# Performance work log

Measured on AMD Instinct MI355X. Metric: run time of the kernel, lower is better.

The kernel has to match this reference:

```python
import jax, jax.numpy as jnp
import numpy as np

# Model config (matches init_kwargs)
DAG_DEPTH = 16
HIDDEN = 2048
B, T = 4, 4096
N = DAG_DEPTH                 # total_nodes
INIT_SLOTS = DAG_DEPTH // 2   # initial slots
INTER = DAG_DEPTH // 2        # intermediate slots / scan steps
LOG_CLAMP = 23.026
SIGN_TEMP = 1e-4


def _xavier(k, shape):
    fan_out, fan_in = shape
    lim = np.sqrt(6.0 / (fan_in + fan_out)).astype(np.float32)
    return jax.random.uniform(k, shape, jnp.float32, -lim, lim)


def setup_inputs() -> dict:
    key = jax.random.key(0)
    k0, k1, k2, k3 = jax.random.split(key, 4)
    return {
        "hidden": jax.random.normal(k0, (B, T, HIDDEN), jnp.float32),
        "W_init": _xavier(k1, (2 * N, HIDDEN)),
        "b_init": jnp.zeros((2 * N,), jnp.float32),
        "W_op": _xavier(k2, (INTER * N, HIDDEN)),
        "b_op": jnp.zeros((INTER * N,), jnp.float32),
        "W_gate": _xavier(k3, (INTER, HIDDEN)),
        "b_gate": jnp.zeros((INTER,), jnp.float32),
    }


def reference(hidden, W_init, b_init, W_op, b_op, W_gate, b_gate):
    Bb, Tt, H = hidden.shape
    # --- plan predictor ---
    init_raw = jnp.einsum('bth,oh->bto', hidden, W_init) + b_init        # (B,T,2N)
    V_mag = jnp.abs(init_raw[..., :N])                                   # (B,T,N)
    V_sign = jnp.tanh(init_raw[..., N:])                                 # (B,T,N)
    O = (jnp.einsum('bth,oh->bto', hidden, W_op) + b_op).reshape(Bb, Tt, INTER, N)
    G = jax.nn.sigmoid(jnp.einsum('bth,oh->bto', hidden, W_gate) + b_gate)  # (B,T,INTER)

    # --- sequential DAG execution (fixed INTER steps, vectorized over B,T) ---
    # NOTE: torch casts to float64 (float32 on mps); here we compute in float32,
    # identical math modulo precision (jax x64 is disabled by default).
    pos = jnp.arange(N)
    for step in range(INTER):
        valid = INIT_SLOTS + step
        mask = (pos < valid).astype(hidden.dtype)                        # causal mask over nodes
        O_s = O[:, :, step, :] * mask                                    # (B,T,N)
        G_s = G[:, :, step:step + 1]                                     # (B,T,1)
        signed = V_sign * V_mag
        log_mag = jnp.log(jnp.clip(V_mag, 1e-12))
        mixed = log_mag * (1.0 - G_s) + signed * G_s
        R = jnp.sum(O_s * mixed, axis=-1, keepdims=True)                 # (B,T,1)
        lin_sign = jnp.tanh(R / SIGN_TEMP)
        sign_prod = jnp.prod(V_sign * (jnp.abs(O_s) + 1.0), axis=-1, keepdims=True)
        log_sign = jnp.tanh(sign_prod / SIGN_TEMP)
        Vs_new = G_s * lin_sign + (1.0 - G_s) * log_sign
        Vm_new = G_s * jnp.abs(R) + (1.0 - G_s) * jnp.exp(jnp.clip(R, None, LOG_CLAMP))
        idx = INIT_SLOTS + step
        V_mag = V_mag.at[:, :, idx].set(Vm_new[..., 0])
        V_sign = V_sign.at[:, :, idx].set(Vs_new[..., 0])

    return V_sign[:, :, -1] * V_mag[:, :, -1]                            # (B,T)
```

## Files before the change

### kernel.cpp

```cpp
#include <hip/hip_runtime.h>
#include <math.h>

#define HID    2048
#define NROW   16384
#define NCOL   168
#define BM     64
#define KSTEPS 64
#define NCHUNK 33
#define NELEM  2112
#define BUFB   33792
#define CPD    172
#define NSLOT  16
#define NSTEP  8

typedef short short8 __attribute__((ext_vector_type(8)));
typedef float f32x4  __attribute__((ext_vector_type(4)));
typedef unsigned int u32x4 __attribute__((ext_vector_type(4)));

static __device__ __forceinline__ unsigned pack_hi(unsigned u0, unsigned u1) {
  return __builtin_amdgcn_perm(u1, u0, 0x07060302u);
}

struct Planes { u32x4 p1, p2, p3; };
static __device__ __forceinline__ Planes split8(const float* x) {
  Planes P;
  #pragma unroll
  for (int q = 0; q < 4; ++q) {
    float x0 = x[2*q], x1 = x[2*q+1];
    unsigned u0 = __float_as_uint(x0), u1 = __float_as_uint(x1);
    P.p1[q] = pack_hi(u0, u1);
    float r0 = x0 - __uint_as_float(u0 & 0xFFFF0000u);
    float r1 = x1 - __uint_as_float(u1 & 0xFFFF0000u);
    unsigned v0 = __float_as_uint(r0), v1 = __float_as_uint(r1);
    P.p2[q] = pack_hi(v0, v1);
    float s0 = r0 - __uint_as_float(v0 & 0xFFFF0000u);
    float s1 = r1 - __uint_as_float(v1 & 0xFFFF0000u);
    P.p3[q] = pack_hi(__float_as_uint(s0), __float_as_uint(s1));
  }
  return P;
}

static __device__ __forceinline__ void loadA8(const float* p, float* x) {
  float4 a = *(const float4*)p;
  float4 b = *(const float4*)(p + 4);
  x[0]=a.x; x[1]=a.y; x[2]=a.z; x[3]=a.w;
  x[4]=b.x; x[5]=b.y; x[6]=b.z; x[7]=b.w;
}

static __device__ __forceinline__ f32x4 mf(short8 a, short8 b, f32x4 c) {
  return __builtin_amdgcn_mfma_f32_16x16x32_bf16(a, b, c, 0, 0, 0);
}

static __device__ __forceinline__ void gld_lds16(const void* g, void* l) {
  __builtin_amdgcn_global_load_lds(
      (const __attribute__((address_space(1))) unsigned int*)g,
      (__attribute__((address_space(3))) unsigned int*)l, 16, 0, 0);
}

__global__ void prep_b(const float* __restrict__ Wi, const float* __restrict__ Wo,
                       const float* __restrict__ Wg, u32x4* __restrict__ wsB) {
  int bid  = blockIdx.x;
  int kidx = bid / 11;
  int nt   = bid - kidx * 11;
  int l    = threadIdx.x;
  int col  = nt * 16 + (l & 15);
  int k0   = kidx * 32 + (l >> 4) * 8;

  float x[8];
  if (col < NCOL) {
    const float* wr = (col < 32)  ? (Wi + (size_t)col * HID)
                    : (col < 160) ? (Wo + (size_t)(col - 32) * HID)
                                  : (Wg + (size_t)(col - 160) * HID);
    loadA8(wr + k0, x);
  } else {
    #pragma unroll
    for (int i = 0; i < 8; ++i) x[i] = 0.f;
  }
  Planes P = split8(x);
  size_t base = (size_t)kidx * NELEM + (nt * 3) * 64 + l;
  wsB[base]       = P.p1;
  wsB[base + 64]  = P.p2;
  wsB[base + 128] = P.p3;
}

__global__ __launch_bounds__(512, 2)
void dag_main(const float* __restrict__ hidden, const u32x4* __restrict__ wsB,
              const float* __restrict__ b_init, const float* __restrict__ b_op,
              const float* __restrict__ b_gate, float* __restrict__ out)
{
  __shared__ __align__(16) char smem[2 * BUFB];

  const int tid = threadIdx.x;
  const int l   = tid & 63;
  const int w   = tid >> 6;
  const int wm  = w >> 2;
  const int wn  = w & 3;
  const int row0 = blockIdx.x * BM;
  const int r   = l & 15;
  const int kg  = l >> 4;

  const float* ap0 = hidden + (size_t)(row0 + wm * 32 + r) * HID + kg * 8;
  const float* ap1 = ap0 + (size_t)16 * HID;

  const u32x4* bsrc = wsB + tid;
  char* wbase = smem + w * 1024;
  const char* brd0 = smem + (wn * 9 * 64 + l) * 16;

  f32x4 acc[2][3];
  const f32x4 zf = {0.f, 0.f, 0.f, 0.f};
  #pragma unroll
  for (int mt = 0; mt < 2; ++mt)
    #pragma unroll
    for (int j = 0; j < 3; ++j) acc[mt][j] = zf;

  float xs0[8], xs1[8];

#define STAGE(t_, sel_) do {                                   \
    const u32x4* s_ = bsrc + (size_t)NELEM * (t_);             \
    char* d_ = wbase + (sel_) * BUFB;                          \
    gld_lds16(s_,        d_);                                  \
    gld_lds16(s_ + 512,  d_ + 8192);                           \
    gld_lds16(s_ + 1024, d_ + 16384);                          \
    gld_lds16(s_ + 1536, d_ + 24576);                          \
    if (w == 0) gld_lds16(s_ + 2048, d_ + 32768 - w * 1024);   \
  } while (0)

  STAGE(0, 0);
  loadA8(ap0, xs0);
  loadA8(ap1, xs1);
  __syncthreads();

  for (int t = 0; t < KSTEPS; ++t) {
    Planes PA0 = split8(xs0);
    Planes PA1 = split8(xs1);
    short8 a0p1 = __builtin_bit_cast(short8, PA0.p1);
    short8 a0p2 = __builtin_bit_cast(short8, PA0.p2);
    short8 a0p3 = __builtin_bit_cast(short8, PA0.p3);
    short8 a1p1 = __builtin_bit_cast(short8, PA1.p1);
    short8 a1p2 = __builtin_bit_cast(short8, PA1.p2);
    short8 a1p3 = __builtin_bit_cast(short8, PA1.p3);

    if (t + 1 < KSTEPS) {
      STAGE(t + 1, (t + 1) & 1);
      loadA8(ap0 + (t + 1) * 32, xs0);
      loadA8(ap1 + (t + 1) * 32, xs1);
    }

    const char* bb = brd0 + (t & 1) * BUFB;
    #pragma unroll
    for (int j = 0; j < 3; ++j) {
      if (wn == 3 && j == 2) continue;
      short8 b1 = *(const short8*)(bb + (j * 3 + 0) * 1024);
      short8 b2 = *(const short8*)(bb + (j * 3 + 1) * 1024);
      short8 b3 = *(const short8*)(bb + (j * 3 + 2) * 1024);
      {
        f32x4 c = acc[0][j];
        c = mf(a0p1, b1, c); c = mf(a0p1, b2, c); c = mf(a0p2, b1, c);
        c = mf(a0p1, b3, c); c = mf(a0p2, b2, c); c = mf(a0p3, b1, c);
        acc[0][j] = c;
      }
      {
        f32x4 c = acc[1][j];
        c = mf(a1p1, b1, c); c = mf(a1p1, b2, c); c = mf(a1p2, b1, c);
        c = mf(a1p1, b3, c); c = mf(a1p2, b2, c); c = mf(a1p3, b1, c);
        acc[1][j] = c;
      }
    }
    __syncthreads();
  }
#undef STAGE

  float (*sC)[CPD] = (float(*)[CPD])smem;
  #pragma unroll
  for (int mt = 0; mt < 2; ++mt) {
    #pragma unroll
    for (int j = 0; j < 3; ++j) {
      int col = wn * 48 + j * 16 + r;
      if (col < NCOL) {
        int row = wm * 32 + mt * 16 + kg * 4;
        sC[row + 0][col] = acc[mt][j][0];
        sC[row + 1][col] = acc[mt][j][1];
        sC[row + 2][col] = acc[mt][j][2];
        sC[row + 3][col] = acc[mt][j][3];
      }
    }
  }
  __syncthreads();

  if (tid < BM) {
    const int rr = tid;
    float Vm[NSLOT], Vs[NSLOT];
    #pragma unroll
    for (int i = 0; i < NSLOT; ++i) {
      float mv = sC[rr][i]      + b_init[i];
      float sv = sC[rr][16 + i] + b_init[16 + i];
      Vm[i] = fabsf(mv);
      Vs[i] = tanhf(sv);
    }
    float G[NSTEP];
    #pragma unroll
    for (int s = 0; s < NSTEP; ++s) {
      float gr = sC[rr][160 + s] + b_gate[s];
      G[s] = 1.0f / (1.0f + expf(-gr));
    }
    #pragma unroll
    for (int s = 0; s < NSTEP; ++s) {
      const float g = G[s];
      float R = 0.f, sp = 1.f;
      #pragma unroll
      for (int i = 0; i < NSLOT; ++i) {
        float Osi = (i < 8 + s) ? (sC[rr][32 + s * 16 + i] + b_op[s * 16 + i]) : 0.f;
        float sgn   = Vs[i] * Vm[i];
        float logm  = logf(fmaxf(Vm[i], 1e-12f));
        float mixed = logm * (1.f - g) + sgn * g;
        R  += Osi * mixed;
        sp *= Vs[i] * (fabsf(Osi) + 1.f);
      }
      float lin_sign = tanhf(R  / 1e-4f);
      float log_sign = tanhf(sp / 1e-4f);
      float vs_new = g * lin_sign + (1.f - g) * log_sign;
      float vm_new = g * fabsf(R) + (1.f - g) * expf(fminf(R, 23.026f));
      Vm[8 + s] = vm_new;
      Vs[8 + s] = vs_new;
    }
    out[row0 + rr] = Vs[NSLOT - 1] * Vm[NSLOT - 1];
  }
}

extern "C" void kernel_launch(void* const* d_in, const int* in_sizes, int n_in,
                              void* d_out, int out_size, void* d_ws, size_t ws_size,
                              hipStream_t stream) {
  (void)in_sizes; (void)n_in; (void)out_size; (void)ws_size;
  const float* hidden = (const float*)d_in[0];
  const float* W_init = (const float*)d_in[1];
  const float* b_init = (const float*)d_in[2];
  const float* W_op   = (const float*)d_in[3];
  const float* b_op   = (const float*)d_in[4];
  const float* W_gate = (const float*)d_in[5];
  const float* b_gate = (const float*)d_in[6];
  float* out = (float*)d_out;
  u32x4* wsB = (u32x4*)d_ws;

  prep_b<<<dim3(704), dim3(64), 0, stream>>>(W_init, W_op, W_gate, wsB);
  dag_main<<<dim3(NROW / BM), dim3(512), 0, stream>>>(hidden, wsB, b_init, b_op,
                                                      b_gate, out);
}
```

Measured before the change: 118.7 us.

## Load B operand directly into registers, drop LDS staging and per-step barriers

Replaces the shared-memory double buffer for the pre-split weight planes, filled with global_load_lds, with per-wave register double buffering. Each wave now loads its own B fragments straight from global memory (L2-resident), which removes the per-iteration __syncthreads and LDS traffic. The K loop is unrolled by two with ping-pong register sets, hidden loads become nontemporal, and s_setprio raises priority around the MFMA block. The cost is more VGPRs, which may hurt occupancy at launch bounds 512x2. Each B fragment is also now fetched separately by the two waves sharing a column group, adding redundant global/L2 traffic.

```diff
diff --git a/kernel.cpp b/kernel.cpp
--- a/kernel.cpp
+++ b/kernel.cpp
@@ -6,9 +6,7 @@
 #define NCOL   168
 #define BM     64
 #define KSTEPS 64
-#define NCHUNK 33
 #define NELEM  2112
-#define BUFB   33792
 #define CPD    172
 #define NSLOT  16
 #define NSTEP  8
@@ -41,20 +39,21 @@
 }
 
 static __device__ __forceinline__ void loadA8(const float* p, float* x) {
-  float4 a = *(const float4*)p;
-  float4 b = *(const float4*)(p + 4);
-  x[0]=a.x; x[1]=a.y; x[2]=a.z; x[3]=a.w;
-  x[4]=b.x; x[5]=b.y; x[6]=b.z; x[7]=b.w;
+  f32x4 a = *(const f32x4*)p;
+  f32x4 b = *(const f32x4*)(p + 4);
+  x[0]=a[0]; x[1]=a[1]; x[2]=a[2]; x[3]=a[3];
+  x[4]=b[0]; x[5]=b[1]; x[6]=b[2]; x[7]=b[3];
+}
+
+static __device__ __forceinline__ void loadA8_nt(const float* p, float* x) {
+  f32x4 a = __builtin_nontemporal_load((const f32x4*)p);
+  f32x4 b = __builtin_nontemporal_load((const f32x4*)(p + 4));
+  x[0]=a[0]; x[1]=a[1]; x[2]=a[2]; x[3]=a[3];
+  x[4]=b[0]; x[5]=b[1]; x[6]=b[2]; x[7]=b[3];
 }
 
 static __device__ __forceinline__ f32x4 mf(short8 a, short8 b, f32x4 c) {
   return __builtin_amdgcn_mfma_f32_16x16x32_bf16(a, b, c, 0, 0, 0);
-}
-
-static __device__ __forceinline__ void gld_lds16(const void* g, void* l) {
-  __builtin_amdgcn_global_load_lds(
-      (const __attribute__((address_space(1))) unsigned int*)g,
-      (__attribute__((address_space(3))) unsigned int*)l, 16, 0, 0);
 }
 
 __global__ void prep_b(const float* __restrict__ Wi, const float* __restrict__ Wo,
@@ -88,7 +87,7 @@
               const float* __restrict__ b_init, const float* __restrict__ b_op,
               const float* __restrict__ b_gate, float* __restrict__ out)
 {
-  __shared__ __align__(16) char smem[2 * BUFB];
+  __shared__ float sC[BM][CPD];
 
   const int tid = threadIdx.x;
   const int l   = tid & 63;
@@ -102,9 +101,7 @@
   const float* ap0 = hidden + (size_t)(row0 + wm * 32 + r) * HID + kg * 8;
   const float* ap1 = ap0 + (size_t)16 * HID;
 
-  const u32x4* bsrc = wsB + tid;
-  char* wbase = smem + w * 1024;
-  const char* brd0 = smem + (wn * 9 * 64 + l) * 16;
+  const u32x4* bbase = wsB + (size_t)(wn * 9) * 64 + l;
 
   f32x4 acc[2][3];
   const f32x4 zf = {0.f, 0.f, 0.f, 0.f};
@@ -113,64 +110,68 @@
     #pragma unroll
     for (int j = 0; j < 3; ++j) acc[mt][j] = zf;
 
-  float xs0[8], xs1[8];
-
-#define STAGE(t_, sel_) do {                                   \
-    const u32x4* s_ = bsrc + (size_t)NELEM * (t_);             \
-    char* d_ = wbase + (sel_) * BUFB;                          \
-    gld_lds16(s_,        d_);                                  \
-    gld_lds16(s_ + 512,  d_ + 8192);                           \
-    gld_lds16(s_ + 1024, d_ + 16384);                          \
-    gld_lds16(s_ + 1536, d_ + 24576);                          \
-    if (w == 0) gld_lds16(s_ + 2048, d_ + 32768 - w * 1024);   \
+  float xc0[8], xc1[8], xn0[8], xn1[8];
+  u32x4 bc[9], bn[9];
+
+#define LOADB(dst_, t_) do {                                   \
+    const u32x4* s_ = bbase + (size_t)NELEM * (t_);            \
+    dst_[0] = s_[0 * 64]; dst_[1] = s_[1 * 64];                \
+    dst_[2] = s_[2 * 64]; dst_[3] = s_[3 * 64];                \
+    dst_[4] = s_[4 * 64]; dst_[5] = s_[5 * 64];                \
+    if (wn != 3) {                                             \
+      dst_[6] = s_[6 * 64]; dst_[7] = s_[7 * 64];              \
+      dst_[8] = s_[8 * 64];                                    \
+    }                                                          \
   } while (0)
 
-  STAGE(0, 0);
-  loadA8(ap0, xs0);
-  loadA8(ap1, xs1);
-  __syncthreads();
-
-  for (int t = 0; t < KSTEPS; ++t) {
-    Planes PA0 = split8(xs0);
-    Planes PA1 = split8(xs1);
-    short8 a0p1 = __builtin_bit_cast(short8, PA0.p1);
-    short8 a0p2 = __builtin_bit_cast(short8, PA0.p2);
-    short8 a0p3 = __builtin_bit_cast(short8, PA0.p3);
-    short8 a1p1 = __builtin_bit_cast(short8, PA1.p1);
-    short8 a1p2 = __builtin_bit_cast(short8, PA1.p2);
-    short8 a1p3 = __builtin_bit_cast(short8, PA1.p3);
-
-    if (t + 1 < KSTEPS) {
-      STAGE(t + 1, (t + 1) & 1);
-      loadA8(ap0 + (t + 1) * 32, xs0);
-      loadA8(ap1 + (t + 1) * 32, xs1);
-    }
-
-    const char* bb = brd0 + (t & 1) * BUFB;
-    #pragma unroll
-    for (int j = 0; j < 3; ++j) {
-      if (wn == 3 && j == 2) continue;
-      short8 b1 = *(const short8*)(bb + (j * 3 + 0) * 1024);
-      short8 b2 = *(const short8*)(bb + (j * 3 + 1) * 1024);
-      short8 b3 = *(const short8*)(bb + (j * 3 + 2) * 1024);
-      {
-        f32x4 c = acc[0][j];
-        c = mf(a0p1, b1, c); c = mf(a0p1, b2, c); c = mf(a0p2, b1, c);
-        c = mf(a0p1, b3, c); c = mf(a0p2, b2, c); c = mf(a0p3, b1, c);
-        acc[0][j] = c;
-      }
-      {
-        f32x4 c = acc[1][j];
-        c = mf(a1p1, b1, c); c = mf(a1p1, b2, c); c = mf(a1p2, b1, c);
-        c = mf(a1p1, b3, c); c = mf(a1p2, b2, c); c = mf(a1p3, b1, c);
-        acc[1][j] = c;
-      }
-    }
-    __syncthreads();
-  }
-#undef STAGE
-
-  float (*sC)[CPD] = (float(*)[CPD])smem;
+#define STEP(bcur_, bnxt_, x0c_, x1c_, x0n_, x1n_, t_) do {                 \
+    Planes PA0 = split8(x0c_);                                              \
+    Planes PA1 = split8(x1c_);                                              \
+    short8 a0p1 = __builtin_bit_cast(short8, PA0.p1);                       \
+    short8 a0p2 = __builtin_bit_cast(short8, PA0.p2);                       \
+    short8 a0p3 = __builtin_bit_cast(short8, PA0.p3);                       \
+    short8 a1p1 = __builtin_bit_cast(short8, PA1.p1);                       \
+    short8 a1p2 = __builtin_bit_cast(short8, PA1.p2);                       \
+    short8 a1p3 = __builtin_bit_cast(short8, PA1.p3);                       \
+    if ((t_) + 1 < KSTEPS) {                                                \
+      loadA8_nt(ap0 + ((t_) + 1) * 32, x0n_);                               \
+      loadA8_nt(ap1 + ((t_) + 1) * 32, x1n_);                               \
+      LOADB(bnxt_, (t_) + 1);                                               \
+    }                                                                       \
+    __builtin_amdgcn_s_setprio(1);                                          \
+    _Pragma("unroll")                                                       \
+    for (int j = 0; j < 3; ++j) {                                           \
+      if (wn == 3 && j == 2) continue;                                      \
+      short8 b1 = __builtin_bit_cast(short8, bcur_[j * 3 + 0]);             \
+      short8 b2 = __builtin_bit_cast(short8, bcur_[j * 3 + 1]);             \
+      short8 b3 = __builtin_bit_cast(short8, bcur_[j * 3 + 2]);             \
+      {                                                                     \
+        f32x4 c = acc[0][j];                                                \
+        c = mf(a0p1, b1, c); c = mf(a0p1, b2, c); c = mf(a0p2, b1, c);      \
+        c = mf(a0p1, b3, c); c = mf(a0p2, b2, c); c = mf(a0p3, b1, c);      \
+        acc[0][j] = c;                                                      \
+      }                                                                     \
+      {                                                                     \
+        f32x4 c = acc[1][j];                                                \
+        c = mf(a1p1, b1, c); c = mf(a1p1, b2, c); c = mf(a1p2, b1, c);      \
+        c = mf(a1p1, b3, c); c = mf(a1p2, b2, c); c = mf(a1p3, b1, c);      \
+        acc[1][j] = c;                                                      \
+      }                                                                     \
+    }                                                                       \
+    __builtin_amdgcn_s_setprio(0);                                          \
+  } while (0)
+
+  loadA8_nt(ap0, xc0);
+  loadA8_nt(ap1, xc1);
+  LOADB(bc, 0);
+
+  for (int t = 0; t < KSTEPS; t += 2) {
+    STEP(bc, bn, xc0, xc1, xn0, xn1, t);
+    STEP(bn, bc, xn0, xn1, xc0, xc1, t + 1);
+  }
+#undef STEP
+#undef LOADB
+
   #pragma unroll
   for (int mt = 0; mt < 2; ++mt) {
     #pragma unroll
```

Measured after the change: 160.4 us. +35.2%, slower.

## Double k-step superstages with explicit vmcnt waits and wave-owned B staging

Applied to the files above, without the earlier changes.

The K loop now runs as 32 superstages, each covering two 32-wide k slices, in place of 64 single steps. Each wave stages only the B chunks it reads, using an explicit vmcnt wait plus a raw s_barrier instead of a full __syncthreads each step. A-operand registers are double buffered, B fragments are loaded into registers before the MFMAs, and setprio raises wave priority during the MFMA block. The aim is to halve barrier count and overlap global-to-LDS loads with compute. In exchange LDS use doubles to about 132KB per block, which likely limits occupancy to one block per CU. Correctness also depends on the hand-set vmcnt being right.

```diff
diff --git a/kernel.cpp b/kernel.cpp
--- a/kernel.cpp
+++ b/kernel.cpp
@@ -6,9 +6,10 @@
 #define NCOL   168
 #define BM     64
 #define KSTEPS 64
-#define NCHUNK 33
+#define NSUP   32
 #define NELEM  2112
-#define BUFB   33792
+#define SLICE  33792
+#define SUPB   67584
 #define CPD    172
 #define NSLOT  16
 #define NSTEP  8
@@ -16,6 +17,10 @@
 typedef short short8 __attribute__((ext_vector_type(8)));
 typedef float f32x4  __attribute__((ext_vector_type(4)));
 typedef unsigned int u32x4 __attribute__((ext_vector_type(4)));
+
+static __device__ __forceinline__ void wait_vm8() {
+  asm volatile("s_waitcnt vmcnt(8)" ::: "memory");
+}
 
 static __device__ __forceinline__ unsigned pack_hi(unsigned u0, unsigned u1) {
   return __builtin_amdgcn_perm(u1, u0, 0x07060302u);
@@ -41,10 +46,10 @@
 }
 
 static __device__ __forceinline__ void loadA8(const float* p, float* x) {
-  float4 a = *(const float4*)p;
-  float4 b = *(const float4*)(p + 4);
-  x[0]=a.x; x[1]=a.y; x[2]=a.z; x[3]=a.w;
-  x[4]=b.x; x[5]=b.y; x[6]=b.z; x[7]=b.w;
+  f32x4 a = *(const f32x4*)p;
+  f32x4 b = *(const f32x4*)(p + 4);
+  x[0]=a[0]; x[1]=a[1]; x[2]=a[2]; x[3]=a[3];
+  x[4]=b[0]; x[5]=b[1]; x[6]=b[2]; x[7]=b[3];
 }
 
 static __device__ __forceinline__ f32x4 mf(short8 a, short8 b, f32x4 c) {
@@ -88,13 +93,13 @@
               const float* __restrict__ b_init, const float* __restrict__ b_op,
               const float* __restrict__ b_gate, float* __restrict__ out)
 {
-  __shared__ __align__(16) char smem[2 * BUFB];
+  __shared__ __align__(16) char smem[2 * SUPB];
 
   const int tid = threadIdx.x;
   const int l   = tid & 63;
   const int w   = tid >> 6;
+  const int wn  = w & 3;
   const int wm  = w >> 2;
-  const int wn  = w & 3;
   const int row0 = blockIdx.x * BM;
   const int r   = l & 15;
   const int kg  = l >> 4;
@@ -102,9 +107,15 @@
   const float* ap0 = hidden + (size_t)(row0 + wm * 32 + r) * HID + kg * 8;
   const float* ap1 = ap0 + (size_t)16 * HID;
 
-  const u32x4* bsrc = wsB + tid;
-  char* wbase = smem + w * 1024;
-  const char* brd0 = smem + (wn * 9 * 64 + l) * 16;
+  const int cb = 9 * wn + (wm ? ((wn == 3) ? 1 : 4) : 0);
+  const u32x4* gsrc[5];
+  char* ldst[5];
+  #pragma unroll
+  for (int i = 0; i < 5; ++i) {
+    gsrc[i] = wsB + (size_t)(cb + i) * 64 + l;
+    ldst[i] = smem + (cb + i) * 1024;
+  }
+  const char* brd0 = smem + (size_t)(9 * wn) * 1024 + (size_t)l * 16;
 
   f32x4 acc[2][3];
   const f32x4 zf = {0.f, 0.f, 0.f, 0.f};
@@ -113,63 +124,85 @@
     #pragma unroll
     for (int j = 0; j < 3; ++j) acc[mt][j] = zf;
 
-  float xs0[8], xs1[8];
-
-#define STAGE(t_, sel_) do {                                   \
-    const u32x4* s_ = bsrc + (size_t)NELEM * (t_);             \
-    char* d_ = wbase + (sel_) * BUFB;                          \
-    gld_lds16(s_,        d_);                                  \
-    gld_lds16(s_ + 512,  d_ + 8192);                           \
-    gld_lds16(s_ + 1024, d_ + 16384);                          \
-    gld_lds16(s_ + 1536, d_ + 24576);                          \
-    if (w == 0) gld_lds16(s_ + 2048, d_ + 32768 - w * 1024);   \
+  float xe0[8], xe1[8], xo0[8], xo1[8];
+
+#define STAGE(s_, sel_) do {                                                 \
+    _Pragma("unroll")                                                        \
+    for (int q = 0; q < 2; ++q)                                              \
+      _Pragma("unroll")                                                      \
+      for (int i = 0; i < 5; ++i)                                            \
+        gld_lds16(gsrc[i] + (size_t)NELEM * (2 * (s_) + q),                  \
+                  ldst[i] + (sel_) * SUPB + q * SLICE);                      \
   } while (0)
 
+#define KSTEP(bb_, xc0_, xc1_, ISSA_, t2_) do {                              \
+    short8 bf[9];                                                            \
+    _Pragma("unroll")                                                        \
+    for (int i = 0; i < 9; ++i)                                              \
+      if (wn != 3 || i < 6) bf[i] = *(const short8*)((bb_) + i * 1024);      \
+    Planes PA0 = split8(xc0_);                                               \
+    Planes PA1 = split8(xc1_);                                               \
+    if (ISSA_) {                                                             \
+      loadA8(ap0 + (t2_) * 32, xc0_);                                        \
+      loadA8(ap1 + (t2_) * 32, xc1_);                                        \
+    }                                                                        \
+    short8 a0p1 = __builtin_bit_cast(short8, PA0.p1);                        \
+    short8 a0p2 = __builtin_bit_cast(short8, PA0.p2);                        \
+    short8 a0p3 = __builtin_bit_cast(short8, PA0.p3);                        \
+    short8 a1p1 = __builtin_bit_cast(short8, PA1.p1);                        \
+    short8 a1p2 = __builtin_bit_cast(short8, PA1.p2);                        \
+    short8 a1p3 = __builtin_bit_cast(short8, PA1.p3);                        \
+    __builtin_amdgcn_s_setprio(1);                                           \
+    _Pragma("unroll")                                                        \
+    for (int j = 0; j < 3; ++j) {                                            \
+      if (wn == 3 && j == 2) continue;                                       \
+      short8 b1 = bf[j * 3 + 0];                                             \
+      short8 b2 = bf[j * 3 + 1];                                             \
+      short8 b3 = bf[j * 3 + 2];                                             \
+      {                                                                      \
+        f32x4 c = acc[0][j];                                                 \
+        c = mf(a0p1, b1, c); c = mf(a0p1, b2, c); c = mf(a0p2, b1, c);       \
+        c = mf(a0p1, b3, c); c = mf(a0p2, b2, c); c = mf(a0p3, b1, c);       \
+        acc[0][j] = c;                                                       \
+      }                                                                      \
+      {                                                                      \
+        f32x4 c = acc[1][j];                                                 \
+        c = mf(a1p1, b1, c); c = mf(a1p1, b2, c); c = mf(a1p2, b1, c);       \
+        c = mf(a1p1, b3, c); c = mf(a1p2, b2, c); c = mf(a1p3, b1, c);       \
+        acc[1][j] = c;                                                       \
+      }                                                                      \
+    }                                                                        \
+    __builtin_amdgcn_s_setprio(0);                                           \
+  } while (0)
+
+#define BODY(s_, p_, ISSUE_) do {                                            \
+    wait_vm8();                                                              \
+    __builtin_amdgcn_sched_barrier(0);                                       \
+    __builtin_amdgcn_s_barrier();                                            \
+    __builtin_amdgcn_sched_barrier(0);                                       \
+    if (ISSUE_) STAGE((s_) + 1, (p_) ^ 1);                                   \
+    const char* be = brd0 + (p_) * SUPB;                                     \
+    KSTEP(be,         xe0, xe1, (ISSUE_), 2 * (s_) + 2);                     \
+    KSTEP(be + SLICE, xo0, xo1, (ISSUE_), 2 * (s_) + 3);                     \
+  } while (0)
+
   STAGE(0, 0);
-  loadA8(ap0, xs0);
-  loadA8(ap1, xs1);
+  loadA8(ap0,      xe0);
+  loadA8(ap1,      xe1);
+  loadA8(ap0 + 32, xo0);
+  loadA8(ap1 + 32, xo1);
+
+  for (int s = 0; s < 30; s += 2) {
+    BODY(s,     0, true);
+    BODY(s + 1, 1, true);
+  }
+  BODY(30, 0, true);
+  BODY(31, 1, false);
+#undef BODY
+#undef KSTEP
+#undef STAGE
+
   __syncthreads();
-
-  for (int t = 0; t < KSTEPS; ++t) {
-    Planes PA0 = split8(xs0);
-    Planes PA1 = split8(xs1);
-    short8 a0p1 = __builtin_bit_cast(short8, PA0.p1);
-    short8 a0p2 = __builtin_bit_cast(short8, PA0.p2);
-    short8 a0p3 = __builtin_bit_cast(short8, PA0.p3);
-    short8 a1p1 = __builtin_bit_cast(short8, PA1.p1);
-    short8 a1p2 = __builtin_bit_cast(short8, PA1.p2);
-    short8 a1p3 = __builtin_bit_cast(short8, PA1.p3);
-
-    if (t + 1 < KSTEPS) {
-      STAGE(t + 1, (t + 1) & 1);
-      loadA8(ap0 + (t + 1) * 32, xs0);
-      loadA8(ap1 + (t + 1) * 32, xs1);
-    }
-
-    const char* bb = brd0 + (t & 1) * BUFB;
-    #pragma unroll
-    for (int j = 0; j < 3; ++j) {
-      if (wn == 3 && j == 2) continue;
-      short8 b1 = *(const short8*)(bb + (j * 3 + 0) * 1024);
-      short8 b2 = *(const short8*)(bb + (j * 3 + 1) * 1024);
-      short8 b3 = *(const short8*)(bb + (j * 3 + 2) * 1024);
-      {
-        f32x4 c = acc[0][j];
-        c = mf(a0p1, b1, c); c = mf(a0p1, b2, c); c = mf(a0p2, b1, c);
-        c = mf(a0p1, b3, c); c = mf(a0p2, b2, c); c = mf(a0p3, b1, c);
-        acc[0][j] = c;
-      }
-      {
-        f32x4 c = acc[1][j];
-        c = mf(a1p1, b1, c); c = mf(a1p1, b2, c); c = mf(a1p2, b1, c);
-        c = mf(a1p1, b3, c); c = mf(a1p2, b2, c); c = mf(a1p3, b1, c);
-        acc[1][j] = c;
-      }
-    }
-    __syncthreads();
-  }
-#undef STAGE
-
   float (*sC)[CPD] = (float(*)[CPD])smem;
   #pragma unroll
   for (int mt = 0; mt < 2; ++mt) {
```

Measured after the change: 100.5 us. 1.18x faster.
